# Kernel tuning notes

Measured on AMD Instinct MI355X. Metric: run time of the kernel, lower is better.

## Reference

```python
import jax, jax.numpy as jnp
import numpy as np

_J6 = jnp.array([[0,0,0,0,0,1],[0,0,0,0,-1,0],[0,0,0,1,0,0],
                 [0,0,1,0,0,0],[0,-1,0,0,0,0],[1,0,0,0,0,0]], dtype=jnp.float32)
_PAIRS4 = [(0,1),(0,2),(0,3),(1,2),(1,3),(2,3)]
H = 16  # n_heads

def _ln(x, g, b, eps=1e-5):
    m = jnp.mean(x, axis=-1, keepdims=True)
    v = jnp.var(x, axis=-1, keepdims=True)
    return (x - m) / jnp.sqrt(v + eps) * g + b

def _exterior(p1, p2):
    # Plucker coordinates of the line through p1,p2 in R^4 -> R^6, normalized
    parts = [p1[..., i] * p2[..., j] - p1[..., j] * p2[..., i] for i, j in _PAIRS4]
    L = jnp.stack(parts, axis=-1)
    n = jnp.linalg.norm(L, axis=-1, keepdims=True)
    return L / jnp.maximum(n, 1e-12)

def _iterated_gram_attn(x, Wqkv, bqkv, W1w, W2w, W1r, W2r, Wmv, bmv, Wmg, bmg,
                        mem_scale, iter_mix, decay_logits, Wout, bout):
    B, T, D = x.shape
    dh = D // H
    # ---- standard causal attention branch ----
    qkv = (x @ Wqkv + bqkv).reshape(B, T, 3, H, dh)
    q = jnp.transpose(qkv[:, :, 0], (0, 2, 1, 3))  # bhtd
    k = jnp.transpose(qkv[:, :, 1], (0, 2, 1, 3))
    v = jnp.transpose(qkv[:, :, 2], (0, 2, 1, 3))
    scores = jnp.einsum('bhtd,bhsd->bhts', q, k) * (dh ** -0.5)
    causal = jnp.tril(jnp.ones((T, T), dtype=bool))
    scores = jnp.where(causal, scores, -jnp.inf)
    attn = jax.nn.softmax(scores, axis=-1)  # dropout is eval-mode identity
    seq_out = jnp.einsum('bhts,bhsd->bhtd', attn, v).transpose(0, 2, 1, 3).reshape(B, T, D)
    # ---- Gram memory branch ----
    x_prev = jnp.concatenate([jnp.zeros_like(x[:, :1]), x[:, :-1]], axis=1)
    w1 = (x_prev @ W1w).reshape(B, T, H, 4)
    w2 = (x @ W2w).reshape(B, T, H, 4)
    write_lines = _exterior(w1, w2)                       # (B,T,H,6)
    r1 = (x @ W1r).reshape(B, T, H, 4)
    r2 = (x @ W2r).reshape(B, T, H, 4)
    read_lines = _exterior(r1, r2)                        # (B,T,H,6)
    Jw = jnp.einsum('bthi,ij->bhtj', write_lines, _J6)    # (B,H,T,6)
    rd = jnp.transpose(read_lines, (0, 2, 1, 3))          # (B,H,T,6)
    decays = jax.nn.sigmoid(decay_logits)                 # (H,)
    pos = jnp.arange(T, dtype=x.dtype)
    outer = Jw[..., :, None] * Jw[..., None, :]           # (B,H,T,6,6)
    dinv = (1.0 / jnp.maximum(decays, 1e-6))[:, None] ** pos[None, :]  # (H,T)
    M = jnp.cumsum(outer * dinv[None, :, :, None, None], axis=2)
    M = jnp.concatenate([jnp.zeros_like(M[:, :, :1]), M[:, :, :-1]], axis=2)  # shift: strictly past
    dfwd = decays[:, None] ** pos[None, :]
    M = M * dfwd[None, :, :, None, None]                  # (B,H,T,6,6)
    rdM = jnp.einsum('bhti,bhtij->bhtj', rd, M)
    score_M = jnp.sum(rdM * rd, axis=-1)                  # (B,H,T)
    score_M2 = jnp.sum(rdM * rdM, axis=-1)
    alpha = jax.nn.sigmoid(iter_mix[0])
    mem_score = (1 - alpha) * score_M + alpha * score_M2
    mem_val = x @ Wmv + bmv                               # (B,T,D)
    gate = jax.nn.sigmoid(x @ Wmg + bmg)                  # (B,T,H)
    gated = jax.nn.sigmoid(jnp.transpose(mem_score, (0, 2, 1)) * mem_scale[None, None, :]) * gate
    gated = jnp.mean(gated, axis=-1, keepdims=True)       # (B,T,1)
    return (seq_out + gated * mem_val) @ Wout + bout

def _block(x, ln1_g, ln1_b, Wqkv, bqkv, W1w, W2w, W1r, W2r, Wmv, bmv, Wmg, bmg,
           mem_scale, iter_mix, decay_logits, Wout, bout,
           ln2_g, ln2_b, Wfc, bfc, Wproj, bproj):
    h = _ln(x, ln1_g, ln1_b)
    x = x + _iterated_gram_attn(h, Wqkv, bqkv, W1w, W2w, W1r, W2r, Wmv, bmv,
                                Wmg, bmg, mem_scale, iter_mix, decay_logits, Wout, bout)
    h2 = _ln(x, ln2_g, ln2_b)
    mlp = jax.nn.gelu(h2 @ Wfc + bfc, approximate=False) @ Wproj + bproj
    return x + mlp

def setup_inputs() -> dict:
    key = jax.random.key(0)
    B, T, D = 2, 1024, 1024
    dff = 4 * D
    ks = jax.random.split(key, 16)
    s = 0.02
    inp = {
        'x': jax.random.normal(ks[0], (B, T, D), jnp.float32),
        'ln1_g': jnp.ones((D,), jnp.float32), 'ln1_b': jnp.zeros((D,), jnp.float32),
        'Wqkv': jax.random.normal(ks[1], (D, 3 * D), jnp.float32) * s,
        'bqkv': jnp.zeros((3 * D,), jnp.float32),
        'W1w': jax.random.normal(ks[2], (D, 4 * H), jnp.float32) * s,
        'W2w': jax.random.normal(ks[3], (D, 4 * H), jnp.float32) * s,
        'W1r': jax.random.normal(ks[4], (D, 4 * H), jnp.float32) * s,
        'W2r': jax.random.normal(ks[5], (D, 4 * H), jnp.float32) * s,
        'Wmv': jax.random.normal(ks[6], (D, D), jnp.float32) * s,
        'bmv': jnp.zeros((D,), jnp.float32),
        'Wmg': jax.random.normal(ks[7], (D, H), jnp.float32) * s,
        'bmg': jnp.zeros((H,), jnp.float32),
        'mem_scale': jnp.full((H,), 0.1, jnp.float32),
        'iter_mix': jnp.zeros((1,), jnp.float32),
        'decay_logits': jnp.full((H,), 4.6, jnp.float32) + 0.1 * jax.random.normal(ks[8], (H,), jnp.float32),
        'Wout': jax.random.normal(ks[9], (D, D), jnp.float32) * s,
        'bout': jnp.zeros((D,), jnp.float32),
        'ln2_g': jnp.ones((D,), jnp.float32), 'ln2_b': jnp.zeros((D,), jnp.float32),
        'Wfc': jax.random.normal(ks[10], (D, dff), jnp.float32) * s,
        'bfc': jnp.zeros((dff,), jnp.float32),
        'Wproj': jax.random.normal(ks[11], (dff, D), jnp.float32) * s,
        'bproj': jnp.zeros((D,), jnp.float32),
    }
    return inp

def reference(x, ln1_g, ln1_b, Wqkv, bqkv, W1w, W2w, W1r, W2r, Wmv, bmv, Wmg, bmg,
              mem_scale, iter_mix, decay_logits, Wout, bout,
              ln2_g, ln2_b, Wfc, bfc, Wproj, bproj):
    return _block(x, ln1_g, ln1_b, Wqkv, bqkv, W1w, W2w, W1r, W2r, Wmv, bmv, Wmg, bmg,
                  mem_scale, iter_mix, decay_logits, Wout, bout,
                  ln2_g, ln2_b, Wfc, bfc, Wproj, bproj)
```

## Files before the change

### kernel.cpp

```cpp
#include <hip/hip_runtime.h>
#include <hip/hip_bf16.h>
#include <math.h>

typedef float f32x4 __attribute__((ext_vector_type(4)));
typedef _Float16 f16x8 __attribute__((ext_vector_type(8)));
typedef _Float16 f16x4 __attribute__((ext_vector_type(4)));

#define TT 1024
#define DD 1024
#define QS 4608

typedef __attribute__((address_space(1))) const void gas_void;
typedef __attribute__((address_space(3))) void las_void;
static __device__ __forceinline__ void gl_lds16(const void* g, void* l) {
  __builtin_amdgcn_global_load_lds((gas_void*)g, (las_void*)l, 16, 0, 0);
}

__global__ __launch_bounds__(512) void gemm_t16(
    const _Float16* __restrict__ A, const _Float16* __restrict__ Wt,
    const float* __restrict__ bias, const float* __restrict__ residual,
    void* __restrict__ Cv, int N, int K, int act, int gx, int mode, int ktiles) {
  __shared__ __align__(16) _Float16 As[3][4096];
  __shared__ __align__(16) _Float16 Bs[3][4096];
  const int tid = threadIdx.x;
  const int lane = tid & 63;
  const int wid = tid >> 6;
  const int wr = wid >> 1, wc = wid & 1;
  const int g = lane >> 4, l16 = lane & 15;
  const int cpx = gridDim.x >> 3;
  const int wg = (blockIdx.x & 7) * cpx + (blockIdx.x >> 3);
  const int row0 = (wg / gx) * 128, col0 = (wg % gx) * 128;
  const int kbeg = blockIdx.y * ktiles * 32;

  f32x4 acc[2][4];
#pragma unroll
  for (int m = 0; m < 2; ++m)
#pragma unroll
    for (int n = 0; n < 4; ++n) acc[m][n] = (f32x4){0.f, 0.f, 0.f, 0.f};

  const int srow = tid >> 2;
  const int goff = ((tid & 3) ^ ((srow >> 1) & 3)) << 3;
  const _Float16* agp = A + (size_t)(row0 + srow) * K + kbeg + goff;
  const _Float16* bgp = Wt + (size_t)(col0 + srow) * K + kbeg + goff;
  const int ldst = tid * 16;

  const int prm = (l16 >> 1) & 3;

  gl_lds16(agp, (char*)As[0] + ldst);
  gl_lds16(bgp, (char*)Bs[0] + ldst);
  if (1 < ktiles) {
    gl_lds16(agp + 32, (char*)As[1] + ldst);
    gl_lds16(bgp + 32, (char*)Bs[1] + ldst);
  }

  int cs = 0, ss = 2;
  for (int kt = 0; kt < ktiles; ++kt) {
    if (kt < ktiles - 1) asm volatile("s_waitcnt vmcnt(2)" ::: "memory");
    else                 asm volatile("s_waitcnt vmcnt(0)" ::: "memory");
    __builtin_amdgcn_s_barrier();
    __builtin_amdgcn_sched_barrier(0);
    if (kt + 2 < ktiles) {
      const int kp = (kt + 2) * 32;
      gl_lds16(agp + kp, (char*)As[ss] + ldst);
      gl_lds16(bgp + kp, (char*)Bs[ss] + ldst);
    }
    f16x8 af[2], bf[4];
#pragma unroll
    for (int m = 0; m < 2; ++m) {
      const int r = wr * 32 + m * 16 + l16;
      af[m] = *(const f16x8*)(As[cs] + r * 32 + ((g ^ prm) << 3));
    }
#pragma unroll
    for (int n = 0; n < 4; ++n) {
      const int c = wc * 64 + n * 16 + l16;
      bf[n] = *(const f16x8*)(Bs[cs] + c * 32 + ((g ^ prm) << 3));
    }
#pragma unroll
    for (int m = 0; m < 2; ++m)
#pragma unroll
      for (int n = 0; n < 4; ++n)
        acc[m][n] = __builtin_amdgcn_mfma_f32_16x16x32_f16(af[m], bf[n], acc[m][n], 0, 0, 0);
    cs = (cs == 2) ? 0 : cs + 1;
    ss = (ss == 2) ? 0 : ss + 1;
  }
#pragma unroll
  for (int m = 0; m < 2; ++m) {
#pragma unroll
    for (int n = 0; n < 4; ++n) {
      const int col = col0 + wc * 64 + n * 16 + l16;
      const float bv = (mode != 2 && bias) ? bias[col] : 0.f;
#pragma unroll
      for (int rg = 0; rg < 4; ++rg) {
        const int row = row0 + wr * 32 + m * 16 + g * 4 + rg;
        const size_t off = (size_t)row * N + col;
        float v = acc[m][n][rg] + bv;
        if (act == 1) v = 0.5f * v * (1.f + erff(v * 0.70710678118654752f));
        if (mode == 2) atomicAdd(&((float*)Cv)[off], v);
        else if (mode == 3) ((float*)Cv)[off] = v + residual[off];
        else ((_Float16*)Cv)[off] = (_Float16)v;
      }
    }
  }
}

static __device__ __forceinline__ void trans_tile(const float* __restrict__ W,
    _Float16* __restrict__ WT, int K, int N, int n0, int k0, int tid) {
  __shared__ float tile[64][65];
  const int tn = tid & 63, tk4 = tid >> 6;
#pragma unroll
  for (int it = 0; it < 16; ++it) {
    const int k = k0 + it * 4 + tk4;
    tile[tn][it * 4 + tk4] = W[(size_t)k * N + n0 + tn];
  }
  __syncthreads();
  const int on = tid >> 2, ok = tid & 3;
  f16x8 a, b;
#pragma unroll
  for (int j = 0; j < 8; ++j) {
    a[j] = (_Float16)tile[on][ok * 16 + j];
    b[j] = (_Float16)tile[on][ok * 16 + 8 + j];
  }
  _Float16* dst = WT + (size_t)(n0 + on) * K + k0 + ok * 16;
  *(f16x8*)dst = a;
  *(f16x8*)(dst + 8) = b;
}

__global__ __launch_bounds__(256) void prep_all(
    const float* __restrict__ Wqkv, const float* __restrict__ W1w, const float* __restrict__ W2w,
    const float* __restrict__ W1r, const float* __restrict__ W2r, const float* __restrict__ Wmg,
    const float* __restrict__ Wmv, const float* __restrict__ Wout, const float* __restrict__ Wfc,
    const float* __restrict__ Wproj, const float* __restrict__ bqkv, const float* __restrict__ bmg,
    const float* __restrict__ bmv, _Float16* __restrict__ WmT, _Float16* __restrict__ WoutT,
    _Float16* __restrict__ WfcT, _Float16* __restrict__ WprojT, float* __restrict__ bm) {
  const int id = blockIdx.x;
  const int tid = threadIdx.x;
  if (id < 1152) {
    __shared__ float tile[64][65];
    const int n0 = (id % 72) * 64, k0 = (id / 72) * 64;
    const int tn = tid & 63, tk4 = tid >> 6;
#pragma unroll
    for (int it = 0; it < 16; ++it) {
      const int k = k0 + it * 4 + tk4;
      const int n = n0 + tn;
      float v;
      if (n < 3072) v = Wqkv[(size_t)k * 3072 + n];
      else if (n < 3136) v = W1w[k * 64 + n - 3072];
      else if (n < 3200) v = W2w[k * 64 + n - 3136];
      else if (n < 3264) v = W1r[k * 64 + n - 3200];
      else if (n < 3328) v = W2r[k * 64 + n - 3264];
      else if (n < 3344) v = Wmg[k * 16 + n - 3328];
      else if (n < 3584) v = 0.f;
      else v = Wmv[(size_t)k * 1024 + n - 3584];
      tile[tn][it * 4 + tk4] = v;
    }
    __syncthreads();
    const int on = tid >> 2, ok = tid & 3;
    f16x8 a, b;
#pragma unroll
    for (int j = 0; j < 8; ++j) {
      a[j] = (_Float16)tile[on][ok * 16 + j];
      b[j] = (_Float16)tile[on][ok * 16 + 8 + j];
    }
    _Float16* dst = WmT + (size_t)(n0 + on) * 1024 + k0 + ok * 16;
    *(f16x8*)dst = a;
    *(f16x8*)(dst + 8) = b;
  } else if (id < 1408) {
    const int i2 = id - 1152;
    trans_tile(Wout, WoutT, 1024, 1024, (i2 % 16) * 64, (i2 / 16) * 64, tid);
  } else if (id < 2432) {
    const int i2 = id - 1408;
    trans_tile(Wfc, WfcT, 1024, 4096, (i2 % 64) * 64, (i2 / 64) * 64, tid);
  } else if (id < 3456) {
    const int i2 = id - 2432;
    trans_tile(Wproj, WprojT, 4096, 1024, (i2 % 16) * 64, (i2 / 16) * 64, tid);
  } else {
    const int col = (id - 3456) * 256 + tid;
    if (col < 4608) {
      float b = 0.f;
      if (col < 3072) b = bqkv[col];
      else if (col >= 3328 && col < 3344) b = bmg[col - 3328];
      else if (col >= 3584) b = bmv[col - 3584];
      bm[col] = b;
    }
  }
}

__global__ __launch_bounds__(256) void ln16(const float* __restrict__ in,
    const float* __restrict__ gw, const float* __restrict__ bw, _Float16* __restrict__ out) {
  const int row = blockIdx.x, tid = threadIdx.x;
  const float* x = in + (size_t)row * DD;
  const float4 v = *(const float4*)(x + tid * 4);
  float s = v.x + v.y + v.z + v.w;
  float sq = v.x * v.x + v.y * v.y + v.z * v.z + v.w * v.w;
#pragma unroll
  for (int off = 32; off >= 1; off >>= 1) { s += __shfl_xor(s, off); sq += __shfl_xor(sq, off); }
  __shared__ float red[8];
  const int lane = tid & 63, wv = tid >> 6;
  if (lane == 0) { red[wv] = s; red[4 + wv] = sq; }
  __syncthreads();
  s = red[0] + red[1] + red[2] + red[3];
  sq = red[4] + red[5] + red[6] + red[7];
  const float mean = s * (1.f / 1024.f);
  const float var = sq * (1.f / 1024.f) - mean * mean;
  const float rstd = rsqrtf(var + 1e-5f);
  const float4 g4 = *(const float4*)(gw + tid * 4);
  const float4 b4 = *(const float4*)(bw + tid * 4);
  f16x4 o;
  o[0] = (_Float16)((v.x - mean) * rstd * g4.x + b4.x);
  o[1] = (_Float16)((v.y - mean) * rstd * g4.y + b4.y);
  o[2] = (_Float16)((v.z - mean) * rstd * g4.z + b4.z);
  o[3] = (_Float16)((v.w - mean) * rstd * g4.w + b4.w);
  *(f16x4*)(out + (size_t)row * DD + tid * 4) = o;
}

static __device__ __forceinline__ int swzA(int row, int k) {
  return row * 64 + ((((k >> 3) ^ row) & 7) << 3) + (k & 7);
}
static __device__ __forceinline__ int swzV(int row, int k) {
  return row * 64 + ((((k >> 3) ^ row ^ (row >> 3)) & 7) << 3) + (k & 7);
}

static __device__ __forceinline__ void attn_step(
    const f16x8* qf, f32x4* oacc, float* m, float* l,
    const _Float16* Kl, const _Float16* Vt, _Float16* Plw,
    bool diag, int wq, int g, int l16) {
  f32x4 s[4];
#pragma unroll
  for (int n = 0; n < 4; ++n) s[n] = (f32x4){0.f, 0.f, 0.f, 0.f};
#pragma unroll
  for (int ks = 0; ks < 2; ++ks) {
    f16x8 kf[4];
#pragma unroll
    for (int n = 0; n < 4; ++n) kf[n] = *(const f16x8*)(Kl + swzA(n * 16 + l16, ks * 32 + g * 8));
#pragma unroll
    for (int n = 0; n < 4; ++n)
      s[n] = __builtin_amdgcn_mfma_f32_16x16x32_f16(qf[ks], kf[n], s[n], 0, 0, 0);
  }
  if (diag) {
    const int rloc = wq * 16 + g * 4;
#pragma unroll
    for (int n = 0; n < 4; ++n) {
      const int cloc = n * 16 + l16;
#pragma unroll
      for (int reg = 0; reg < 4; ++reg)
        if (cloc > rloc + reg) s[n][reg] = -INFINITY;
    }
  }
  float f[4];
#pragma unroll
  for (int reg = 0; reg < 4; ++reg) {
    float t = fmaxf(fmaxf(s[0][reg], s[1][reg]), fmaxf(s[2][reg], s[3][reg]));
#pragma unroll
    for (int off = 1; off < 16; off <<= 1) t = fmaxf(t, __shfl_xor(t, off));
    const float nm = fmaxf(m[reg], t);
    f[reg] = __expf(m[reg] - nm);
    m[reg] = nm;
  }
  float rs[4] = {0.f, 0.f, 0.f, 0.f};
#pragma unroll
  for (int n = 0; n < 4; ++n) {
#pragma unroll
    for (int reg = 0; reg < 4; ++reg) {
      const float p = __expf(s[n][reg] - m[reg]);
      rs[reg] += p;
      Plw[swzA(g * 4 + reg, n * 16 + l16)] = (_Float16)p;
    }
  }
#pragma unroll
  for (int reg = 0; reg < 4; ++reg) {
    float t = rs[reg];
#pragma unroll
    for (int off = 1; off < 16; off <<= 1) t += __shfl_xor(t, off);
    l[reg] = l[reg] * f[reg] + t;
  }
#pragma unroll
  for (int n = 0; n < 4; ++n)
#pragma unroll
    for (int reg = 0; reg < 4; ++reg) oacc[n][reg] *= f[reg];
#pragma unroll
  for (int ks = 0; ks < 2; ++ks) {
    const f16x8 pa = *(const f16x8*)(Plw + swzA(l16, ks * 32 + g * 8));
    f16x8 vb[4];
#pragma unroll
    for (int n = 0; n < 4; ++n) vb[n] = *(const f16x8*)(Vt + swzV(n * 16 + l16, ks * 32 + g * 8));
#pragma unroll
    for (int n = 0; n < 4; ++n)
      oacc[n] = __builtin_amdgcn_mfma_f32_16x16x32_f16(pa, vb[n], oacc[n], 0, 0, 0);
  }
}

__global__ __launch_bounds__(256) void attn_mfma(const _Float16* __restrict__ qkv,
                                                 _Float16* __restrict__ seq_out) {
  __shared__ __align__(16) _Float16 Kl[64 * 64];
  __shared__ __align__(16) _Float16 Vt[64 * 64];
  __shared__ __align__(16) _Float16 Pl[4][16 * 64];
  const int tid = threadIdx.x, lane = tid & 63, wq = tid >> 6;
  const int g = lane >> 4, l16 = lane & 15;
  const int p = blockIdx.x, hh = blockIdx.y, bb = blockIdx.z;
  const int qt0 = p, qt1 = 15 - p;
  const int ntt = qt1 + 1;

  f16x8 qf0[2], qf1[2];
  {
    const _Float16* q0 = qkv + (size_t)(bb * TT + qt0 * 64 + wq * 16 + l16) * QS + hh * 64;
    const _Float16* q1 = qkv + (size_t)(bb * TT + qt1 * 64 + wq * 16 + l16) * QS + hh * 64;
#pragma unroll
    for (int ks = 0; ks < 2; ++ks) {
      const f16x8 a0 = *(const f16x8*)(q0 + ks * 32 + g * 8);
      const f16x8 a1 = *(const f16x8*)(q1 + ks * 32 + g * 8);
#pragma unroll
      for (int j = 0; j < 8; ++j) {
        qf0[ks][j] = (_Float16)((float)a0[j] * 0.125f);
        qf1[ks][j] = (_Float16)((float)a1[j] * 0.125f);
      }
    }
  }

  f32x4 oacc0[4], oacc1[4];
#pragma unroll
  for (int n = 0; n < 4; ++n) {
    oacc0[n] = (f32x4){0.f, 0.f, 0.f, 0.f};
    oacc1[n] = (f32x4){0.f, 0.f, 0.f, 0.f};
  }
  float m0[4] = {-INFINITY, -INFINITY, -INFINITY, -INFINITY};
  float l0[4] = {0.f, 0.f, 0.f, 0.f};
  float m1[4] = {-INFINITY, -INFINITY, -INFINITY, -INFINITY};
  float l1[4] = {0.f, 0.f, 0.f, 0.f};

  const int skey = tid >> 2, sc4 = tid & 3;

  for (int tt = 0; tt < ntt; ++tt) {
    if (tt) __syncthreads();
    {
      const _Float16* kp = qkv + (size_t)(bb * TT + tt * 64 + skey) * QS + hh * 64 + 1024;
      const _Float16* vp = kp + 1024;
#pragma unroll
      for (int ii = 0; ii < 4; ++ii) {
        const int d0 = sc4 * 4 + ii * 16;
        *(f16x4*)(Kl + swzA(skey, d0)) = *(const f16x4*)(kp + d0);
        const f16x4 vv = *(const f16x4*)(vp + d0);
        Vt[swzV(d0 + 0, skey)] = vv[0];
        Vt[swzV(d0 + 1, skey)] = vv[1];
        Vt[swzV(d0 + 2, skey)] = vv[2];
        Vt[swzV(d0 + 3, skey)] = vv[3];
      }
    }
    __syncthreads();
    attn_step(qf1, oacc1, m1, l1, Kl, Vt, Pl[wq], tt == qt1, wq, g, l16);
    if (tt <= qt0)
      attn_step(qf0, oacc0, m0, l0, Kl, Vt, Pl[wq], tt == qt0, wq, g, l16);
  }
#pragma unroll
  for (int n = 0; n < 4; ++n) {
#pragma unroll
    for (int reg = 0; reg < 4; ++reg) {
      const int r0 = qt0 * 64 + wq * 16 + g * 4 + reg;
      const int r1 = qt1 * 64 + wq * 16 + g * 4 + reg;
      seq_out[(size_t)(bb * TT + r0) * DD + hh * 64 + n * 16 + l16] = (_Float16)(oacc0[n][reg] / l0[reg]);
      seq_out[(size_t)(bb * TT + r1) * DD + hh * 64 + n * 16 + l16] = (_Float16)(oacc1[n][reg] / l1[reg]);
    }
  }
}

static __device__ __forceinline__ void ext6(const float* a, const float* b, float* L) {
  L[0] = a[0] * b[1] - a[1] * b[0];
  L[1] = a[0] * b[2] - a[2] * b[0];
  L[2] = a[0] * b[3] - a[3] * b[0];
  L[3] = a[1] * b[2] - a[2] * b[1];
  L[4] = a[1] * b[3] - a[3] * b[1];
  L[5] = a[2] * b[3] - a[3] * b[2];
  const float n = sqrtf(L[0]*L[0] + L[1]*L[1] + L[2]*L[2] + L[3]*L[3] + L[4]*L[4] + L[5]*L[5]);
  const float s = 1.f / fmaxf(n, 1e-12f);
#pragma unroll
  for (int i = 0; i < 6; ++i) L[i] *= s;
}

__global__ void lines_post(const _Float16* __restrict__ mega, float* __restrict__ jw,
                           float* __restrict__ rdv, float* __restrict__ gate) {
  const int idx = blockIdx.x * 256 + threadIdx.x;
  const int h = idx & 15;
  const int bt = idx >> 4;
  const int t = bt & 1023;
  const int b = bt >> 10;
  const _Float16* row = mega + (size_t)bt * QS + 3072;
  float w1[4] = {0.f, 0.f, 0.f, 0.f}, w2[4], r1[4], r2[4];
  if (t > 0) {
#pragma unroll
    for (int i = 0; i < 4; ++i) w1[i] = (float)row[-QS + h * 4 + i];
  }
#pragma unroll
  for (int i = 0; i < 4; ++i) {
    w2[i] = (float)row[64 + h * 4 + i];
    r1[i] = (float)row[128 + h * 4 + i];
    r2[i] = (float)row[192 + h * 4 + i];
  }
  const float gp = (float)row[256 + h];
  float wl[6], rl[6];
  ext6(w1, w2, wl);
  ext6(r1, r2, rl);
  const size_t o = ((size_t)(b * 16 + h) * 1024 + t) * 6;
  jw[o + 0] =  wl[5]; jw[o + 1] = -wl[4]; jw[o + 2] =  wl[3];
  jw[o + 3] =  wl[2]; jw[o + 4] = -wl[1]; jw[o + 5] =  wl[0];
#pragma unroll
  for (int i = 0; i < 6; ++i) rdv[o + i] = rl[i];
  gate[idx] = 1.f / (1.f + __expf(-gp));
}

static __device__ __forceinline__ int midx(int i, int j) {
  return (i <= j) ? (i * (13 - i)) / 2 + (j - i) : (j * (13 - j)) / 2 + (i - j);
}

__global__ __launch_bounds__(64) void gram_scan(const float* __restrict__ jwv,
    const float* __restrict__ rdv, const float* __restrict__ decay_logits,
    const float* __restrict__ iter_mix, float* __restrict__ mem_score) {
  const int h = blockIdx.x & 15, b = blockIdx.x >> 4;
  const int lane = threadIdx.x;
  const float decay = 1.f / (1.f + __expf(-decay_logits[h]));
  const float alpha = 1.f / (1.f + __expf(-iter_mix[0]));
  __shared__ float sd[64 * 193];
  const size_t base = (size_t)(b * 16 + h) * 1024 * 6;
  for (int it = 0; it < 96; ++it) {
    const int idx = it * 64 + lane;
    const int t = idx / 6, i = idx - 6 * t;
    const int ld = t >> 4, s = t & 15;
    sd[ld * 193 + s * 6 + i] = jwv[base + idx];
    sd[ld * 193 + 96 + s * 6 + i] = rdv[base + idx];
  }
  __syncthreads();
  const float* seg = sd + lane * 193;

  float C[21];
#pragma unroll
  for (int e = 0; e < 21; ++e) C[e] = 0.f;
  for (int s = 0; s < 16; ++s) {
    float J[6], dJ[6];
#pragma unroll
    for (int i = 0; i < 6; ++i) { J[i] = seg[s * 6 + i]; dJ[i] = decay * J[i]; }
#pragma unroll
    for (int i = 0; i < 6; ++i)
#pragma unroll
      for (int j = i; j < 6; ++j)
        C[midx(i, j)] = decay * C[midx(i, j)] + dJ[i] * J[j];
  }
  const float d2 = decay * decay, d4 = d2 * d2, d8 = d4 * d4;
  float fk = d8 * d8;
#pragma unroll
  for (int k = 0; k < 6; ++k) {
    const int off = 1 << k;
#pragma unroll
    for (int e = 0; e < 21; ++e) {
      const float u = __shfl(C[e], lane - off);
      if (lane >= off) C[e] += fk * u;
    }
    fk = fk * fk;
  }
  float M[21];
#pragma unroll
  for (int e = 0; e < 21; ++e) {
    const float u = __shfl(C[e], lane - 1);
    M[e] = (lane >= 1) ? u : 0.f;
  }
  float* msp = mem_score + (size_t)(b * 16 + h) * 1024 + lane * 16;
  for (int s = 0; s < 16; ++s) {
    float J[6], r[6];
#pragma unroll
    for (int i = 0; i < 6; ++i) { J[i] = seg[s * 6 + i]; r[i] = seg[96 + s * 6 + i]; }
    float rdM[6];
#pragma unroll
    for (int i = 0; i < 6; ++i) {
      float a = 0.f;
#pragma unroll
      for (int j = 0; j < 6; ++j) a += M[midx(i, j)] * r[j];
      rdM[i] = a;
    }
    float s1 = 0.f, s2 = 0.f;
#pragma unroll
    for (int i = 0; i < 6; ++i) { s1 += rdM[i] * r[i]; s2 += rdM[i] * rdM[i]; }
    msp[s] = (1.f - alpha) * s1 + alpha * s2;
    float dJ[6];
#pragma unroll
    for (int i = 0; i < 6; ++i) dJ[i] = decay * J[i];
#pragma unroll
    for (int i = 0; i < 6; ++i)
#pragma unroll
      for (int j = i; j < 6; ++j)
        M[midx(i, j)] = decay * M[midx(i, j)] + dJ[i] * J[j];
  }
}

__global__ __launch_bounds__(256) void combine_kernel(const _Float16* __restrict__ seq,
    const _Float16* __restrict__ mega, const float* __restrict__ ms,
    const float* __restrict__ gate, const float* __restrict__ mem_scale,
    _Float16* __restrict__ outp) {
  const int bt = blockIdx.x;
  const int b = bt >> 10, t = bt & 1023;
  __shared__ float hterm[16];
  const int tid = threadIdx.x;
  if (tid < 16) {
    const float sc = ms[(size_t)(b * 16 + tid) * 1024 + t];
    const float gt = gate[(size_t)bt * 16 + tid];
    hterm[tid] = (1.f / (1.f + __expf(-sc * mem_scale[tid]))) * gt;
  }
  __syncthreads();
  float acc = 0.f;
#pragma unroll
  for (int h = 0; h < 16; ++h) acc += hterm[h];
  const float g = acc * (1.f / 16.f);
  const f16x4 s4 = *(const f16x4*)(seq + (size_t)bt * 1024 + tid * 4);
  const f16x4 m4 = *(const f16x4*)(mega + (size_t)bt * QS + 3584 + tid * 4);
  f16x4 o;
#pragma unroll
  for (int j = 0; j < 4; ++j) o[j] = (_Float16)((float)s4[j] + g * (float)m4[j]);
  *(f16x4*)(outp + (size_t)bt * 1024 + tid * 4) = o;
}

__global__ void addb_init(const float* __restrict__ src, const float* __restrict__ bias,
                          float* __restrict__ dst) {
  const size_t i = (size_t)blockIdx.x * 256 + threadIdx.x;
  const int c4 = (int)(i & 255);
  const float4 s = ((const float4*)src)[i];
  const float4 b = ((const float4*)bias)[c4];
  float4 o;
  o.x = s.x + b.x; o.y = s.y + b.y; o.z = s.z + b.z; o.w = s.w + b.w;
  ((float4*)dst)[i] = o;
}

extern "C" void kernel_launch(void* const* d_in, const int* in_sizes, int n_in,
                              void* d_out, int out_size, void* d_ws, size_t ws_size,
                              hipStream_t stream) {
  (void)in_sizes; (void)n_in; (void)out_size; (void)ws_size;
  const float* x       = (const float*)d_in[0];
  const float* ln1_g   = (const float*)d_in[1];
  const float* ln1_b   = (const float*)d_in[2];
  const float* Wqkv    = (const float*)d_in[3];
  const float* bqkv    = (const float*)d_in[4];
  const float* W1w     = (const float*)d_in[5];
  const float* W2w     = (const float*)d_in[6];
  const float* W1r     = (const float*)d_in[7];
  const float* W2r     = (const float*)d_in[8];
  const float* Wmv     = (const float*)d_in[9];
  const float* bmv     = (const float*)d_in[10];
  const float* Wmg     = (const float*)d_in[11];
  const float* bmg     = (const float*)d_in[12];
  const float* mscale  = (const float*)d_in[13];
  const float* itermix = (const float*)d_in[14];
  const float* dlogits = (const float*)d_in[15];
  const float* Wout    = (const float*)d_in[16];
  const float* bout    = (const float*)d_in[17];
  const float* ln2_g   = (const float*)d_in[18];
  const float* ln2_b   = (const float*)d_in[19];
  const float* Wfc     = (const float*)d_in[20];
  const float* bfc     = (const float*)d_in[21];
  const float* Wproj   = (const float*)d_in[22];
  const float* bproj   = (const float*)d_in[23];
  float* out = (float*)d_out;
  float* ws = (float*)d_ws;

  const size_t M1 = 1u << 20;
  _Float16* h16    = (_Float16*)ws;
  _Float16* WmT    = (_Float16*)(ws + 1 * M1);
  float*    bm     = ws + 3407872;
  float*    jw     = ws + 3538944;
  float*    rd     = ws + 3538944 + 196608;
  float*    gate   = ws + 3538944 + 393216;
  float*    ms     = ws + 3538944 + 425984;
  float*    y      = ws + 4 * M1;
  _Float16* mega   = (_Float16*)(ws + 6 * M1);
  _Float16* fc16   = (_Float16*)(ws + 6 * M1);
  _Float16* seq16  = (_Float16*)(ws + 11010048);
  _Float16* WoutT  = (_Float16*)(ws + 12058624);
  _Float16* WfcT   = (_Float16*)(ws + 12 * M1);
  _Float16* WprojT = (_Float16*)(ws + 14 * M1);

  prep_all<<<3474, 256, 0, stream>>>(Wqkv, W1w, W2w, W1r, W2r, Wmg, Wmv, Wout, Wfc, Wproj,
                                     bqkv, bmg, bmv, WmT, WoutT, WfcT, WprojT, bm);

  ln16<<<2048, 256, 0, stream>>>(x, ln1_g, ln1_b, h16);
  gemm_t16<<<576, 512, 0, stream>>>(h16, WmT, bm, nullptr, mega, 4608, 1024, 0, 36, 1, 32);
  attn_mfma<<<dim3(8, 16, 2), 256, 0, stream>>>(mega, seq16);
  lines_post<<<128, 256, 0, stream>>>(mega, jw, rd, gate);
  gram_scan<<<32, 64, 0, stream>>>(jw, rd, dlogits, itermix, ms);
  combine_kernel<<<2048, 256, 0, stream>>>(seq16, mega, ms, gate, mscale, h16);
  gemm_t16<<<128, 512, 0, stream>>>(h16, WoutT, bout, x, y, 1024, 1024, 0, 8, 3, 32);
  ln16<<<2048, 256, 0, stream>>>(y, ln2_g, ln2_b, h16);
  gemm_t16<<<512, 512, 0, stream>>>(h16, WfcT, bfc, nullptr, fc16, 4096, 1024, 1, 32, 1, 32);
  addb_init<<<2048, 256, 0, stream>>>(y, bproj, out);
  gemm_t16<<<dim3(128, 4), 512, 0, stream>>>(fc16, WprojT, nullptr, nullptr, out, 1024, 4096, 0, 8, 2, 32);
}
```

Baseline: 235.9 us.

## Fuse line extraction into gram scan and deepen GEMM prefetch pipeline to four stages

The separate lines_post kernel is removed. gram_scan now reads the projected coordinates from the mega buffer, builds the Plucker lines and gate values in LDS, and atomically accumulates the per-token head-averaged gated memory score into a small buffer that prep_all zero-fills. combine_kernel then just reads one scalar per token. Separately, the GEMM goes from a 3-stage to a 4-stage LDS ring with prefetch distance 3, which raises LDS use per block. This removes one launch and the jw/rd/gate/ms round trips, but it puts serial global loads inside a 32-block scan kernel, and the float atomics change the order of the summation.

```diff
diff --git a/kernel.cpp b/kernel.cpp
--- a/kernel.cpp
+++ b/kernel.cpp
@@ -20,8 +20,8 @@
     const _Float16* __restrict__ A, const _Float16* __restrict__ Wt,
     const float* __restrict__ bias, const float* __restrict__ residual,
     void* __restrict__ Cv, int N, int K, int act, int gx, int mode, int ktiles) {
-  __shared__ __align__(16) _Float16 As[3][4096];
-  __shared__ __align__(16) _Float16 Bs[3][4096];
+  __shared__ __align__(16) _Float16 As[4][4096];
+  __shared__ __align__(16) _Float16 Bs[4][4096];
   const int tid = threadIdx.x;
   const int lane = tid & 63;
   const int wid = tid >> 6;
@@ -52,18 +52,25 @@
     gl_lds16(agp + 32, (char*)As[1] + ldst);
     gl_lds16(bgp + 32, (char*)Bs[1] + ldst);
   }
-
-  int cs = 0, ss = 2;
+  if (2 < ktiles) {
+    gl_lds16(agp + 64, (char*)As[2] + ldst);
+    gl_lds16(bgp + 64, (char*)Bs[2] + ldst);
+  }
+
   for (int kt = 0; kt < ktiles; ++kt) {
-    if (kt < ktiles - 1) asm volatile("s_waitcnt vmcnt(2)" ::: "memory");
-    else                 asm volatile("s_waitcnt vmcnt(0)" ::: "memory");
+    const int rem = ktiles - 1 - kt;
+    if (rem >= 2)      asm volatile("s_waitcnt vmcnt(4)" ::: "memory");
+    else if (rem == 1) asm volatile("s_waitcnt vmcnt(2)" ::: "memory");
+    else               asm volatile("s_waitcnt vmcnt(0)" ::: "memory");
     __builtin_amdgcn_s_barrier();
     __builtin_amdgcn_sched_barrier(0);
-    if (kt + 2 < ktiles) {
-      const int kp = (kt + 2) * 32;
-      gl_lds16(agp + kp, (char*)As[ss] + ldst);
-      gl_lds16(bgp + kp, (char*)Bs[ss] + ldst);
-    }
+    if (kt + 3 < ktiles) {
+      const int kp = (kt + 3) * 32;
+      const int b4 = (kt + 3) & 3;
+      gl_lds16(agp + kp, (char*)As[b4] + ldst);
+      gl_lds16(bgp + kp, (char*)Bs[b4] + ldst);
+    }
+    const int cs = kt & 3;
     f16x8 af[2], bf[4];
 #pragma unroll
     for (int m = 0; m < 2; ++m) {
@@ -80,8 +87,6 @@
 #pragma unroll
       for (int n = 0; n < 4; ++n)
         acc[m][n] = __builtin_amdgcn_mfma_f32_16x16x32_f16(af[m], bf[n], acc[m][n], 0, 0, 0);
-    cs = (cs == 2) ? 0 : cs + 1;
-    ss = (ss == 2) ? 0 : ss + 1;
   }
 #pragma unroll
   for (int m = 0; m < 2; ++m) {
@@ -131,7 +136,8 @@
     const float* __restrict__ Wmv, const float* __restrict__ Wout, const float* __restrict__ Wfc,
     const float* __restrict__ Wproj, const float* __restrict__ bqkv, const float* __restrict__ bmg,
     const float* __restrict__ bmv, _Float16* __restrict__ WmT, _Float16* __restrict__ WoutT,
-    _Float16* __restrict__ WfcT, _Float16* __restrict__ WprojT, float* __restrict__ bm) {
+    _Float16* __restrict__ WfcT, _Float16* __restrict__ WprojT, float* __restrict__ bm,
+    float* __restrict__ gm) {
   const int id = blockIdx.x;
   const int tid = threadIdx.x;
   if (id < 1152) {
@@ -173,7 +179,7 @@
   } else if (id < 3456) {
     const int i2 = id - 2432;
     trans_tile(Wproj, WprojT, 4096, 1024, (i2 % 16) * 64, (i2 / 16) * 64, tid);
-  } else {
+  } else if (id < 3474) {
     const int col = (id - 3456) * 256 + tid;
     if (col < 4608) {
       float b = 0.f;
@@ -182,6 +188,8 @@
       else if (col >= 3584) b = bmv[col - 3584];
       bm[col] = b;
     }
+  } else {
+    gm[(id - 3474) * 256 + tid] = 0.f;
   }
 }
 
@@ -362,6 +370,9 @@
   }
 }
 
+static __device__ __forceinline__ int midx(int i, int j) {
+  return (i <= j) ? (i * (13 - i)) / 2 + (j - i) : (j * (13 - j)) / 2 + (i - j);
+}
 static __device__ __forceinline__ void ext6(const float* a, const float* b, float* L) {
   L[0] = a[0] * b[1] - a[1] * b[0];
   L[1] = a[0] * b[2] - a[2] * b[0];
@@ -375,59 +386,42 @@
   for (int i = 0; i < 6; ++i) L[i] *= s;
 }
 
-__global__ void lines_post(const _Float16* __restrict__ mega, float* __restrict__ jw,
-                           float* __restrict__ rdv, float* __restrict__ gate) {
-  const int idx = blockIdx.x * 256 + threadIdx.x;
-  const int h = idx & 15;
-  const int bt = idx >> 4;
-  const int t = bt & 1023;
-  const int b = bt >> 10;
-  const _Float16* row = mega + (size_t)bt * QS + 3072;
-  float w1[4] = {0.f, 0.f, 0.f, 0.f}, w2[4], r1[4], r2[4];
-  if (t > 0) {
-#pragma unroll
-    for (int i = 0; i < 4; ++i) w1[i] = (float)row[-QS + h * 4 + i];
-  }
-#pragma unroll
-  for (int i = 0; i < 4; ++i) {
-    w2[i] = (float)row[64 + h * 4 + i];
-    r1[i] = (float)row[128 + h * 4 + i];
-    r2[i] = (float)row[192 + h * 4 + i];
-  }
-  const float gp = (float)row[256 + h];
-  float wl[6], rl[6];
-  ext6(w1, w2, wl);
-  ext6(r1, r2, rl);
-  const size_t o = ((size_t)(b * 16 + h) * 1024 + t) * 6;
-  jw[o + 0] =  wl[5]; jw[o + 1] = -wl[4]; jw[o + 2] =  wl[3];
-  jw[o + 3] =  wl[2]; jw[o + 4] = -wl[1]; jw[o + 5] =  wl[0];
-#pragma unroll
-  for (int i = 0; i < 6; ++i) rdv[o + i] = rl[i];
-  gate[idx] = 1.f / (1.f + __expf(-gp));
-}
-
-static __device__ __forceinline__ int midx(int i, int j) {
-  return (i <= j) ? (i * (13 - i)) / 2 + (j - i) : (j * (13 - j)) / 2 + (i - j);
-}
-
-__global__ __launch_bounds__(64) void gram_scan(const float* __restrict__ jwv,
-    const float* __restrict__ rdv, const float* __restrict__ decay_logits,
-    const float* __restrict__ iter_mix, float* __restrict__ mem_score) {
+__global__ __launch_bounds__(64) void gram_scan(const _Float16* __restrict__ mega,
+    const float* __restrict__ decay_logits, const float* __restrict__ iter_mix,
+    const float* __restrict__ mem_scale, float* __restrict__ gm) {
   const int h = blockIdx.x & 15, b = blockIdx.x >> 4;
   const int lane = threadIdx.x;
   const float decay = 1.f / (1.f + __expf(-decay_logits[h]));
   const float alpha = 1.f / (1.f + __expf(-iter_mix[0]));
-  __shared__ float sd[64 * 193];
-  const size_t base = (size_t)(b * 16 + h) * 1024 * 6;
-  for (int it = 0; it < 96; ++it) {
-    const int idx = it * 64 + lane;
-    const int t = idx / 6, i = idx - 6 * t;
-    const int ld = t >> 4, s = t & 15;
-    sd[ld * 193 + s * 6 + i] = jwv[base + idx];
-    sd[ld * 193 + 96 + s * 6 + i] = rdv[base + idx];
-  }
-  __syncthreads();
-  const float* seg = sd + lane * 193;
+  const float msc = mem_scale[h];
+  __shared__ float sd[64 * 209];
+  float* seg = sd + lane * 209;
+  const int tbase = lane * 16;
+
+  for (int s = 0; s < 16; ++s) {
+    const int t = tbase + s;
+    const _Float16* row = mega + (size_t)(b * TT + t) * QS + 3072;
+    float w1[4] = {0.f, 0.f, 0.f, 0.f}, w2[4], r1[4], r2[4];
+    if (t > 0) {
+#pragma unroll
+      for (int i = 0; i < 4; ++i) w1[i] = (float)row[-QS + h * 4 + i];
+    }
+#pragma unroll
+    for (int i = 0; i < 4; ++i) {
+      w2[i] = (float)row[64 + h * 4 + i];
+      r1[i] = (float)row[128 + h * 4 + i];
+      r2[i] = (float)row[192 + h * 4 + i];
+    }
+    const float gp = (float)row[256 + h];
+    float wl[6], rl[6];
+    ext6(w1, w2, wl);
+    ext6(r1, r2, rl);
+    seg[s * 6 + 0] =  wl[5]; seg[s * 6 + 1] = -wl[4]; seg[s * 6 + 2] =  wl[3];
+    seg[s * 6 + 3] =  wl[2]; seg[s * 6 + 4] = -wl[1]; seg[s * 6 + 5] =  wl[0];
+#pragma unroll
+    for (int i = 0; i < 6; ++i) seg[96 + s * 6 + i] = rl[i];
+    seg[192 + s] = 1.f / (1.f + __expf(-gp));
+  }
 
   float C[21];
 #pragma unroll
@@ -460,7 +454,7 @@
     const float u = __shfl(C[e], lane - 1);
     M[e] = (lane >= 1) ? u : 0.f;
   }
-  float* msp = mem_score + (size_t)(b * 16 + h) * 1024 + lane * 16;
+  float* gmp = gm + b * TT + tbase;
   for (int s = 0; s < 16; ++s) {
     float J[6], r[6];
 #pragma unroll
@@ -476,7 +470,9 @@
     float s1 = 0.f, s2 = 0.f;
 #pragma unroll
     for (int i = 0; i < 6; ++i) { s1 += rdM[i] * r[i]; s2 += rdM[i] * rdM[i]; }
-    msp[s] = (1.f - alpha) * s1 + alpha * s2;
+    const float score = (1.f - alpha) * s1 + alpha * s2;
+    const float val = (1.f / (1.f + __expf(-score * msc))) * seg[192 + s];
+    atomicAdd(&gmp[s], val * (1.f / 16.f));
     float dJ[6];
 #pragma unroll
     for (int i = 0; i < 6; ++i) dJ[i] = decay * J[i];
@@ -488,30 +484,17 @@
   }
 }
 
-__global__ __launch_bounds__(256) void combine_kernel(const _Float16* __restrict__ seq,
-    const _Float16* __restrict__ mega, const float* __restrict__ ms,
-    const float* __restrict__ gate, const float* __restrict__ mem_scale,
-    _Float16* __restrict__ outp) {
-  const int bt = blockIdx.x;
-  const int b = bt >> 10, t = bt & 1023;
-  __shared__ float hterm[16];
-  const int tid = threadIdx.x;
-  if (tid < 16) {
-    const float sc = ms[(size_t)(b * 16 + tid) * 1024 + t];
-    const float gt = gate[(size_t)bt * 16 + tid];
-    hterm[tid] = (1.f / (1.f + __expf(-sc * mem_scale[tid]))) * gt;
-  }
-  __syncthreads();
-  float acc = 0.f;
-#pragma unroll
-  for (int h = 0; h < 16; ++h) acc += hterm[h];
-  const float g = acc * (1.f / 16.f);
-  const f16x4 s4 = *(const f16x4*)(seq + (size_t)bt * 1024 + tid * 4);
-  const f16x4 m4 = *(const f16x4*)(mega + (size_t)bt * QS + 3584 + tid * 4);
+__global__ void combine_kernel(const _Float16* __restrict__ seq, const _Float16* __restrict__ mega,
+    const float* __restrict__ gm, _Float16* __restrict__ outp) {
+  const int i = blockIdx.x * 256 + threadIdx.x;
+  const int bt = i >> 8, c4 = i & 255;
+  const float g = gm[bt];
+  const f16x4 s4 = *(const f16x4*)(seq + (size_t)i * 4);
+  const f16x4 m4 = *(const f16x4*)(mega + (size_t)bt * QS + 3584 + c4 * 4);
   f16x4 o;
 #pragma unroll
   for (int j = 0; j < 4; ++j) o[j] = (_Float16)((float)s4[j] + g * (float)m4[j]);
-  *(f16x4*)(outp + (size_t)bt * 1024 + tid * 4) = o;
+  *(f16x4*)(outp + (size_t)i * 4) = o;
 }
 
 __global__ void addb_init(const float* __restrict__ src, const float* __restrict__ bias,
@@ -560,10 +543,7 @@
   _Float16* h16    = (_Float16*)ws;
   _Float16* WmT    = (_Float16*)(ws + 1 * M1);
   float*    bm     = ws + 3407872;
-  float*    jw     = ws + 3538944;
-  float*    rd     = ws + 3538944 + 196608;
-  float*    gate   = ws + 3538944 + 393216;
-  float*    ms     = ws + 3538944 + 425984;
+  float*    gm     = ws + 3538944;
   float*    y      = ws + 4 * M1;
   _Float16* mega   = (_Float16*)(ws + 6 * M1);
   _Float16* fc16   = (_Float16*)(ws + 6 * M1);
@@ -572,15 +552,14 @@
   _Float16* WfcT   = (_Float16*)(ws + 12 * M1);
   _Float16* WprojT = (_Float16*)(ws + 14 * M1);
 
-  prep_all<<<3474, 256, 0, stream>>>(Wqkv, W1w, W2w, W1r, W2r, Wmg, Wmv, Wout, Wfc, Wproj,
-                                     bqkv, bmg, bmv, WmT, WoutT, WfcT, WprojT, bm);
+  prep_all<<<3482, 256, 0, stream>>>(Wqkv, W1w, W2w, W1r, W2r, Wmg, Wmv, Wout, Wfc, Wproj,
+                                     bqkv, bmg, bmv, WmT, WoutT, WfcT, WprojT, bm, gm);
 
   ln16<<<2048, 256, 0, stream>>>(x, ln1_g, ln1_b, h16);
   gemm_t16<<<576, 512, 0, stream>>>(h16, WmT, bm, nullptr, mega, 4608, 1024, 0, 36, 1, 32);
   attn_mfma<<<dim3(8, 16, 2), 256, 0, stream>>>(mega, seq16);
-  lines_post<<<128, 256, 0, stream>>>(mega, jw, rd, gate);
-  gram_scan<<<32, 64, 0, stream>>>(jw, rd, dlogits, itermix, ms);
-  combine_kernel<<<2048, 256, 0, stream>>>(seq16, mega, ms, gate, mscale, h16);
+  gram_scan<<<32, 64, 0, stream>>>(mega, dlogits, itermix, mscale, gm);
+  combine_kernel<<<2048, 256, 0, stream>>>(seq16, mega, gm, h16);
   gemm_t16<<<128, 512, 0, stream>>>(h16, WoutT, bout, x, y, 1024, 1024, 0, 8, 3, 32);
   ln16<<<2048, 256, 0, stream>>>(y, ln2_g, ln2_b, h16);
   gemm_t16<<<512, 512, 0, stream>>>(h16, WfcT, bfc, nullptr, fc16, 4096, 1024, 1, 32, 1, 32);
```

Result: slower. 256.5 us (+8.8%).
